# Optimization experiments

Measured on AMD Instinct MI355X. Metric: run time of the kernel, lower is better.

## Reference

```python
import jax, jax.numpy as jnp
import numpy as np

B, N, D = 8, 1024, 768
H, Y, M = 12, 64, 3072  # heads, head_dim, hopfield memories (4*D)
STEPS = 12
ALPHA = 0.1
EPS = 1e-5


def setup_inputs() -> dict:
    key = jax.random.key(0)
    k0, k1, k2, k3 = jax.random.split(key, 4)
    return {
        "x": jax.random.normal(k0, (B, N, D), dtype=jnp.float32),
        "gamma": jnp.ones((D,), dtype=jnp.float32),
        "beta_ln": jnp.zeros((D,), dtype=jnp.float32),
        "Wq": jax.random.normal(k1, (H, Y, D), dtype=jnp.float32) / np.float32(np.sqrt(D)),
        "Wk": jax.random.normal(k2, (H, Y, D), dtype=jnp.float32) / np.float32(np.sqrt(D)),
        "xi": jax.random.normal(k3, (M, D), dtype=jnp.float32) / np.float32(np.sqrt(D)),
    }


def _layernorm(x, gamma, beta_ln):
    mu = jnp.mean(x, axis=-1, keepdims=True)
    var = jnp.var(x, axis=-1, keepdims=True)
    return gamma * (x - mu) * jax.lax.rsqrt(var + EPS) + beta_ln


def _energy(g, Wq, Wk, xi):
    # Energy attention: E^ATT = -(1/beta) * sum_{h,q} logsumexp_k(beta * <K_hk, Q_hq>)
    q = jnp.einsum('hyd,bnd->bhny', Wq, g)
    k = jnp.einsum('hyd,bnd->bhny', Wk, g)
    beta = jnp.asarray(1.0 / np.sqrt(Y), g.dtype)
    scores = beta * jnp.einsum('bhky,bhqy->bhkq', k, q)  # [B,H,N_k,N_q]
    e_att = -(1.0 / beta) * jnp.sum(jax.nn.logsumexp(scores, axis=2))
    # Hopfield energy: E^HN = -0.5 * sum relu(g @ xi^T)^2
    h = jnp.einsum('bnd,md->bnm', g, xi)
    e_hn = -0.5 * jnp.sum(jnp.square(jax.nn.relu(h)))
    return e_att + e_hn


def reference(x, gamma, beta_ln, Wq, Wk, xi):
    grad_e = jax.grad(_energy)
    def step(xc, _):
        g = _layernorm(xc, gamma, beta_ln)
        # gradient taken at g (not chained through LayerNorm), then SGD update
        xc = xc - ALPHA * grad_e(g, Wq, Wk, xi)
        return xc, None
    out, _ = jax.lax.scan(step, x, None, length=STEPS)
    return out
```

## Files before the change

### kernel.cpp

```cpp
#include <hip/hip_runtime.h>
#include <math.h>

#define H_ 12
#define STEPS_ 12
#define ALPHA_ 0.1f
#define EPS_ 1e-5f
#define BETA_ 0.125f
#define NTOK 8192

typedef unsigned short u16;
typedef __attribute__((ext_vector_type(8))) u16 u16x8;
typedef __attribute__((ext_vector_type(4))) u16 u16x4;
typedef __attribute__((ext_vector_type(4))) float f32x4;
typedef __attribute__((ext_vector_type(8))) __bf16 bf16x8;

#define MFMA __builtin_amdgcn_mfma_f32_16x16x32_bf16

__device__ __forceinline__ u16 f2bf(float x) {
    unsigned u = __float_as_uint(x);
    u += 0x7FFFu + ((u >> 16) & 1u);
    return (u16)(u >> 16);
}
__device__ __forceinline__ float bf2f(u16 u) {
    return __uint_as_float(((unsigned)u) << 16);
}

__device__ __forceinline__ void gl2lds16(const u16* gsrc, u16* ldst) {
    __builtin_amdgcn_global_load_lds(
        (const __attribute__((address_space(1))) void*)gsrc,
        (__attribute__((address_space(3))) void*)ldst, 16, 0, 0);
}

#define RAW_BARRIER()   asm volatile("s_barrier" ::: "memory")
#define WAIT_VM(n)      asm volatile("s_waitcnt vmcnt(" #n ")" ::: "memory")
#define SCHED_FENCE()   __builtin_amdgcn_sched_barrier(0)

#define QUAD(IB, JB, BR) \
    { _Pragma("unroll") \
      for (int i_ = 0; i_ < 4; ++i_) { \
        _Pragma("unroll") \
        for (int j_ = 0; j_ < 2; ++j_) { \
            acc[(IB)+i_][(JB)+j_] = MFMA(afr[i_][0], BR[j_][0], acc[(IB)+i_][(JB)+j_], 0,0,0); \
            acc[(IB)+i_][(JB)+j_] = MFMA(afr[i_][1], BR[j_][1], acc[(IB)+i_][(JB)+j_], 0,0,0); \
        } } }

__global__ __launch_bounds__(256) void ln_kernel(const float* __restrict__ x,
    const float* __restrict__ gamma, const float* __restrict__ beta,
    u16* __restrict__ g)
{
    int row = blockIdx.x;
    const float* xr = x + (size_t)row * 768;
    u16* gr = g + (size_t)row * 768;
    int t = threadIdx.x;
    float v0 = xr[t], v1 = xr[t + 256], v2 = xr[t + 512];
    float s = v0 + v1 + v2;
    #pragma unroll
    for (int off = 32; off > 0; off >>= 1) s += __shfl_down(s, off);
    __shared__ float red[8];
    int wid = t >> 6, lane = t & 63;
    if (lane == 0) red[wid] = s;
    __syncthreads();
    if (t == 0) red[0] = (red[0] + red[1] + red[2] + red[3]) * (1.0f / 768.0f);
    __syncthreads();
    float mu = red[0];
    float d0 = v0 - mu, d1 = v1 - mu, d2 = v2 - mu;
    float ss = d0*d0 + d1*d1 + d2*d2;
    #pragma unroll
    for (int off = 32; off > 0; off >>= 1) ss += __shfl_down(ss, off);
    if (lane == 0) red[4 + wid] = ss;
    __syncthreads();
    if (t == 0) red[4] = rsqrtf((red[4] + red[5] + red[6] + red[7]) * (1.0f / 768.0f) + EPS_);
    __syncthreads();
    float rs = red[4];
    gr[t]       = f2bf(gamma[t]       * d0 * rs + beta[t]);
    gr[t + 256] = f2bf(gamma[t + 256] * d1 * rs + beta[t + 256]);
    gr[t + 512] = f2bf(gamma[t + 512] * d2 * rs + beta[t + 512]);
}

__global__ __launch_bounds__(192) void reduce_ln(const u16* __restrict__ part,
    float* __restrict__ xc, const float* __restrict__ gamma,
    const float* __restrict__ beta, u16* __restrict__ g)
{
    int row = blockIdx.x, t = threadIdx.x;
    const u16x4* p0 = (const u16x4*)(part + (size_t)row * 768);
    const u16x4* p1 = (const u16x4*)(part + (size_t)(8192 + row) * 768);
    const u16x4* p2 = (const u16x4*)(part + (size_t)(16384 + row) * 768);
    const u16x4* p3 = (const u16x4*)(part + (size_t)(24576 + row) * 768);
    f32x4* xr = (f32x4*)(xc + (size_t)row * 768);
    f32x4 v = xr[t];
    u16x4 a = p0[t], b = p1[t], c = p2[t], d4 = p3[t];
    #pragma unroll
    for (int e = 0; e < 4; ++e)
        v[e] = fmaf(ALPHA_, (bf2f(a[e]) + bf2f(b[e])) + (bf2f(c[e]) + bf2f(d4[e])), v[e]);
    xr[t] = v;
    float s = (v[0] + v[1]) + (v[2] + v[3]);
    #pragma unroll
    for (int off = 32; off > 0; off >>= 1) s += __shfl_down(s, off);
    __shared__ float red[8];
    int wid = t >> 6, lane = t & 63;
    if (lane == 0) red[wid] = s;
    __syncthreads();
    if (t == 0) red[0] = (red[0] + red[1] + red[2]) * (1.0f / 768.0f);
    __syncthreads();
    float mu = red[0];
    f32x4 d;
    #pragma unroll
    for (int e = 0; e < 4; ++e) d[e] = v[e] - mu;
    float ss = (d[0]*d[0] + d[1]*d[1]) + (d[2]*d[2] + d[3]*d[3]);
    #pragma unroll
    for (int off = 32; off > 0; off >>= 1) ss += __shfl_down(ss, off);
    if (lane == 0) red[4 + wid] = ss;
    __syncthreads();
    if (t == 0) red[4] = rsqrtf((red[4] + red[5] + red[6]) * (1.0f / 768.0f) + EPS_);
    __syncthreads();
    float rs = red[4];
    const f32x4 gm = *(const f32x4*)&gamma[t * 4];
    const f32x4 bt = *(const f32x4*)&beta[t * 4];
    u16x4 o;
    #pragma unroll
    for (int e = 0; e < 4; ++e) o[e] = f2bf(fmaf(gm[e], d[e] * rs, bt[e]));
    *(u16x4*)&g[(size_t)row * 768 + t * 4] = o;
}

__global__ __launch_bounds__(256) void convert_bf(const float* __restrict__ src,
                                                  u16* __restrict__ dst, int n4)
{
    int i = blockIdx.x * 256 + threadIdx.x;
    if (i < n4) {
        f32x4 v = *(const f32x4*)&src[i * 4];
        u16x4 o;
        #pragma unroll
        for (int e = 0; e < 4; ++e) o[e] = f2bf(v[e]);
        *(u16x4*)&dst[i * 4] = o;
    }
}

__global__ __launch_bounds__(256) void transpose_bf(const float* __restrict__ Wq,
    const float* __restrict__ Wk, const float* __restrict__ xi, u16* __restrict__ out)
{
    __shared__ float tile[64][65];
    int rb = blockIdx.x * 64, cb = blockIdx.y * 64;
    const float* src;
    if (rb < 768) src = Wq + (size_t)rb * 768;
    else if (rb < 1536) src = Wk + (size_t)(rb - 768) * 768;
    else src = xi + (size_t)(rb - 1536) * 768;
    int t = threadIdx.x;
    #pragma unroll
    for (int it = 0; it < 4; ++it) {
        int r = (t >> 4) + 16 * it;
        f32x4 v = *(const f32x4*)&src[(size_t)r * 768 + cb + (t & 15) * 4];
        #pragma unroll
        for (int e = 0; e < 4; ++e) tile[r][(t & 15) * 4 + e] = v[e];
    }
    __syncthreads();
    #pragma unroll
    for (int it = 0; it < 4; ++it) {
        int cl = (t >> 4) + 16 * it;
        u16x4 o;
        #pragma unroll
        for (int e = 0; e < 4; ++e) o[e] = f2bf(tile[(t & 15) * 4 + e][cl]);
        *(u16x4*)&out[(size_t)(cb + cl) * 4608 + rb + (t & 15) * 4] = o;
    }
}

__global__ __launch_bounds__(512) void gemm_fwd(
    const u16* __restrict__ A,
    const u16* __restrict__ Bt,
    u16* __restrict__ qkb, u16* __restrict__ qkT, u16* __restrict__ midb)
{
    __shared__ __align__(16) u16 S[2][32768];
    const int t = threadIdx.x, w = t >> 6, l = t & 63, g = l >> 4, cid = l & 15;
    const int lr = l & 15, lc = l >> 4;
    const int wm = w >> 2, wn = w & 3;
    const int flat = blockIdx.x;
    const int xcd = flat & 7, slot = flat >> 3;
    const int nid = slot >> 2, mloc = slot & 3;
    const int bm = (xcd * 4 + mloc) * 256;
    const int bn = nid * 256;
    const int NT = 12;

    const u16* aA[2]; const u16* bB[2];
    int ldA[2], ldB[2];
    #pragma unroll
    for (int hh = 0; hh < 2; ++hh) {
        aA[hh] = A  + (size_t)(bm + 16 * (hh * 8 + w) + lr) * 768 + 8 * lc;
        bB[hh] = Bt + (size_t)(bn + 16 * (hh * 8 + w) + lr) * 768 + 8 * lc;
        ldA[hh] = (128 * (hh * 8 + w) + l) * 8;
        ldB[hh] = 16384 + (128 * (hh * 8 + w) + l) * 8;
    }
    auto stageA = [&](int buf, int hh, int k0) {
        gl2lds16(aA[hh] + k0,      &S[buf][ldA[hh]]);
        gl2lds16(aA[hh] + k0 + 32, &S[buf][ldA[hh] + 512]);
    };
    auto stageB = [&](int buf, int hh, int k0) {
        gl2lds16(bB[hh] + k0,      &S[buf][ldB[hh]]);
        gl2lds16(bB[hh] + k0 + 32, &S[buf][ldB[hh] + 512]);
    };

    f32x4 acc[8][4] = {};
    bf16x8 afr[4][2], b0[2][2], b1[2][2];

    stageB(0, 0, 0); stageB(0, 1, 0); stageA(0, 0, 0); stageA(0, 1, 0);
    stageB(1, 0, 64); stageB(1, 1, 64);
    WAIT_VM(4); RAW_BARRIER();

    #pragma unroll 1
    for (int tt = 0; tt < NT; ++tt) {
        const int bf = tt & 1, ob = bf ^ 1;
        const u16* Sa = &S[bf][0];
        const u16* Sb = &S[bf][16384];
        #define LDS_A(ii, hh) (*(const bf16x8*)&Sa[(wm*1024 + (ii)*128 + (hh)*64 + l) * 8])
        #define LDS_B(jj, hh) (*(const bf16x8*)&Sb[((wn*4 + (jj))*128 + (hh)*64 + l) * 8])
        #pragma unroll
        for (int i = 0; i < 4; ++i) { afr[i][0] = LDS_A(i, 0); afr[i][1] = LDS_A(i, 1); }
        #pragma unroll
        for (int j = 0; j < 2; ++j) { b0[j][0] = LDS_B(j, 0); b0[j][1] = LDS_B(j, 1); }
        if (tt + 1 < NT) stageA(ob, 0, 64 * (tt + 1));
        RAW_BARRIER();
        __builtin_amdgcn_s_setprio(1);
        QUAD(0, 0, b0);
        __builtin_amdgcn_s_setprio(0);
        SCHED_FENCE(); RAW_BARRIER();
        #pragma unroll
        for (int j = 0; j < 2; ++j) { b1[j][0] = LDS_B(2 + j, 0); b1[j][1] = LDS_B(2 + j, 1); }
        if (tt + 1 < NT) stageA(ob, 1, 64 * (tt + 1));
        RAW_BARRIER();
        __builtin_amdgcn_s_setprio(1);
        QUAD(0, 2, b1);
        __builtin_amdgcn_s_setprio(0);
        SCHED_FENCE(); RAW_BARRIER();
        #pragma unroll
        for (int i = 0; i < 4; ++i) { afr[i][0] = LDS_A(4 + i, 0); afr[i][1] = LDS_A(4 + i, 1); }
        if (tt + 2 < NT) stageB(bf, 0, 64 * (tt + 2));
        RAW_BARRIER();
        __builtin_amdgcn_s_setprio(1);
        QUAD(4, 2, b1);
        __builtin_amdgcn_s_setprio(0);
        SCHED_FENCE(); RAW_BARRIER();
        if (tt + 2 < NT) stageB(bf, 1, 64 * (tt + 2));
        RAW_BARRIER();
        __builtin_amdgcn_s_setprio(1);
        QUAD(4, 0, b0);
        __builtin_amdgcn_s_setprio(0);
        SCHED_FENCE();
        if (tt < NT - 2)       { WAIT_VM(4); }
        else if (tt == NT - 2) { WAIT_VM(0); }
        RAW_BARRIER();
        #undef LDS_A
        #undef LDS_B
    }

    if (bn < 1536) {
        int bidx = bm >> 10;
        #pragma unroll
        for (int i = 0; i < 8; ++i) {
            int tok = bm + wm * 128 + 16 * i + 4 * g;
            #pragma unroll
            for (int j = 0; j < 4; ++j) {
                int col = bn + wn * 64 + 16 * j + cid;
                int sel = col >= 768 ? 1 : 0;
                int cc = col - 768 * sel;
                int hh = cc >> 6, yy = cc & 63;
                u16x4 tv;
                #pragma unroll
                for (int r = 0; r < 4; ++r) {
                    u16 bv = f2bf(acc[i][j][r]);
                    tv[r] = bv;
                    qkb[(size_t)(tok + r) * 1536 + col] = bv;
                }
                *(u16x4*)&qkT[((((size_t)bidx * 12 + hh) * 2 + sel) * 64 + yy) * 1024 + (tok & 1023)] = tv;
            }
        }
    } else {
        #pragma unroll
        for (int i = 0; i < 8; ++i)
            #pragma unroll
            for (int r = 0; r < 4; ++r) {
                size_t row = bm + wm * 128 + 16 * i + 4 * g + r;
                #pragma unroll
                for (int j = 0; j < 4; ++j) {
                    int col = bn + wn * 64 + 16 * j + cid;
                    midb[row * 4608 + col] = f2bf(fmaxf(acc[i][j][r], 0.0f));
                }
            }
    }
}

__global__ __launch_bounds__(512) void gemm_upd(
    const u16* __restrict__ A,
    const u16* __restrict__ Bt,
    u16* __restrict__ part)
{
    __shared__ __align__(16) u16 S[2][32768];
    const int t = threadIdx.x, w = t >> 6, l = t & 63, g = l >> 4, cid = l & 15;
    const int lr = l & 15, lc = l >> 4;
    const int wm = w >> 2, wn = w & 3;
    const int flat = blockIdx.x;
    const int xcd = flat & 7, slot = flat >> 3;
    const int z = slot / 12, rem = slot % 12;
    const int nid = rem >> 2, mloc = rem & 3;
    const int bm = (xcd * 4 + mloc) * 256, bn = nid * 256;
    const int kbeg = z * 1152;
    const int NT = 18;
    u16* out = part + (size_t)z * 8192 * 768;

    const u16* aA[2]; const u16* bB[2];
    int ldA[2], ldB[2];
    #pragma unroll
    for (int hh = 0; hh < 2; ++hh) {
        aA[hh] = A  + (size_t)(bm + 16 * (hh * 8 + w) + lr) * 4608 + kbeg + 8 * lc;
        bB[hh] = Bt + (size_t)(bn + 16 * (hh * 8 + w) + lr) * 4608 + kbeg + 8 * lc;
        ldA[hh] = (128 * (hh * 8 + w) + l) * 8;
        ldB[hh] = 16384 + (128 * (hh * 8 + w) + l) * 8;
    }
    auto stageA = [&](int buf, int hh, int k0) {
        gl2lds16(aA[hh] + k0,      &S[buf][ldA[hh]]);
        gl2lds16(aA[hh] + k0 + 32, &S[buf][ldA[hh] + 512]);
    };
    auto stageB = [&](int buf, int hh, int k0) {
        gl2lds16(bB[hh] + k0,      &S[buf][ldB[hh]]);
        gl2lds16(bB[hh] + k0 + 32, &S[buf][ldB[hh] + 512]);
    };

    f32x4 acc[8][4] = {};
    bf16x8 afr[4][2], b0[2][2], b1[2][2];

    stageB(0, 0, 0); stageB(0, 1, 0); stageA(0, 0, 0); stageA(0, 1, 0);
    stageB(1, 0, 64); stageB(1, 1, 64);
    WAIT_VM(4); RAW_BARRIER();

    #pragma unroll 1
    for (int tt = 0; tt < NT; ++tt) {
        const int bf = tt & 1, ob = bf ^ 1;
        const u16* Sa = &S[bf][0];
        const u16* Sb = &S[bf][16384];
        #define LDS_A(ii, hh) (*(const bf16x8*)&Sa[(wm*1024 + (ii)*128 + (hh)*64 + l) * 8])
        #define LDS_B(jj, hh) (*(const bf16x8*)&Sb[((wn*4 + (jj))*128 + (hh)*64 + l) * 8])
        #pragma unroll
        for (int i = 0; i < 4; ++i) { afr[i][0] = LDS_A(i, 0); afr[i][1] = LDS_A(i, 1); }
        #pragma unroll
        for (int j = 0; j < 2; ++j) { b0[j][0] = LDS_B(j, 0); b0[j][1] = LDS_B(j, 1); }
        if (tt + 1 < NT) stageA(ob, 0, 64 * (tt + 1));
        RAW_BARRIER();
        __builtin_amdgcn_s_setprio(1);
        QUAD(0, 0, b0);
        __builtin_amdgcn_s_setprio(0);
        SCHED_FENCE(); RAW_BARRIER();
        #pragma unroll
        for (int j = 0; j < 2; ++j) { b1[j][0] = LDS_B(2 + j, 0); b1[j][1] = LDS_B(2 + j, 1); }
        if (tt + 1 < NT) stageA(ob, 1, 64 * (tt + 1));
        RAW_BARRIER();
        __builtin_amdgcn_s_setprio(1);
        QUAD(0, 2, b1);
        __builtin_amdgcn_s_setprio(0);
        SCHED_FENCE(); RAW_BARRIER();
        #pragma unroll
        for (int i = 0; i < 4; ++i) { afr[i][0] = LDS_A(4 + i, 0); afr[i][1] = LDS_A(4 + i, 1); }
        if (tt + 2 < NT) stageB(bf, 0, 64 * (tt + 2));
        RAW_BARRIER();
        __builtin_amdgcn_s_setprio(1);
        QUAD(4, 2, b1);
        __builtin_amdgcn_s_setprio(0);
        SCHED_FENCE(); RAW_BARRIER();
        if (tt + 2 < NT) stageB(bf, 1, 64 * (tt + 2));
        RAW_BARRIER();
        __builtin_amdgcn_s_setprio(1);
        QUAD(4, 0, b0);
        __builtin_amdgcn_s_setprio(0);
        SCHED_FENCE();
        if (tt < NT - 2)       { WAIT_VM(4); }
        else if (tt == NT - 2) { WAIT_VM(0); }
        RAW_BARRIER();
        #undef LDS_A
        #undef LDS_B
    }

    #pragma unroll
    for (int i = 0; i < 8; ++i)
        #pragma unroll
        for (int r = 0; r < 4; ++r) {
            size_t row = bm + wm * 128 + 16 * i + 4 * g + r;
            #pragma unroll
            for (int j = 0; j < 4; ++j)
                out[row * 768 + bn + wn * 64 + 16 * j + cid] = f2bf(acc[i][j][r]);
        }
}

__global__ __launch_bounds__(256) void dq_kernel(const u16* __restrict__ qk,
    const u16* __restrict__ qkT, float* __restrict__ L, u16* __restrict__ mid)
{
    const int flat = blockIdx.x;
    const int xcd = flat & 7, slot = flat >> 3;
    const int bh = xcd * 12 + slot / 8;
    const int q0 = (slot % 8) << 7;
    const int b = bh / H_, h = bh % H_;
    const u16* qbase = qk + (size_t)b * 1024 * 1536 + h * 64;
    const u16* kbase = qbase + 768;
    const u16* ktg = qkT + ((size_t)bh * 2 + 1) * 64 * 1024;
    __shared__ __align__(16) u16 KB[2][8192];
    __shared__ __align__(16) u16 Ps[8192];
    const int t = threadIdx.x, w = t >> 6, l = t & 63, g = l >> 4, cid = l & 15;
    const int lr = l & 15, lc = l >> 4;

    #pragma unroll
    for (int h2 = 0; h2 < 2; ++h2)
        #pragma unroll
        for (int ch = 0; ch < 2; ++ch)
            gl2lds16(&qbase[(size_t)(q0 + 32 * w + 16 * h2 + lr) * 1536 + 32 * ch + 8 * lc],
                     &KB[0][(128 * (2 * w + h2) + 64 * ch + l) * 8]);
    __syncthreads();
    bf16x8 QF[2][2];
    #pragma unroll
    for (int jj = 0; jj < 2; ++jj)
        #pragma unroll
        for (int hh = 0; hh < 2; ++hh)
            QF[jj][hh] = *(const bf16x8*)&KB[0][(128 * (2 * w + jj) + 64 * hh + l) * 8];
    __syncthreads();

    auto stageK = [&](int buf, int kt) {
        #pragma unroll
        for (int ch = 0; ch < 2; ++ch) {
            gl2lds16(&kbase[(size_t)(kt * 64 + 16 * w + lr) * 1536 + 32 * ch + 8 * lc],
                     &KB[buf][(128 * w + 64 * ch + l) * 8]);
            gl2lds16(&ktg[(size_t)(16 * w + lr) * 1024 + kt * 64 + 32 * ch + 8 * lc],
                     &KB[buf][4096 + (128 * w + 64 * ch + l) * 8]);
        }
    };

    f32x4 acc[2][4] = {};
    float lrun[2] = {0.0f, 0.0f};

    stageK(0, 0); stageK(1, 1);
    #pragma unroll 1
    for (int kt = 0; kt < 16; ++kt) {
        if (kt == 15) { WAIT_VM(0); } else { WAIT_VM(4); }
        RAW_BARRIER();
        const int buf = kt & 1;
        const u16* Kn = &KB[buf][0];
        const u16* Kt = &KB[buf][4096];
        f32x4 s[4][2];
        #pragma unroll
        for (int i = 0; i < 4; ++i) {
            bf16x8 a0 = *(const bf16x8*)&Kn[(128 * i + l) * 8];
            bf16x8 a1 = *(const bf16x8*)&Kn[(128 * i + 64 + l) * 8];
            #pragma unroll
            for (int jj = 0; jj < 2; ++jj) {
                f32x4 z = {0.f, 0.f, 0.f, 0.f};
                z = MFMA(a0, QF[jj][0], z, 0, 0, 0);
                z = MFMA(a1, QF[jj][1], z, 0, 0, 0);
                s[i][jj] = z;
            }
        }
        #pragma unroll
        for (int jj = 0; jj < 2; ++jj) {
            float psum = 0.0f;
            #pragma unroll
            for (int i = 0; i < 4; ++i) {
                u16x4 pv;
                #pragma unroll
                for (int r = 0; r < 4; ++r) {
                    float p = __expf(s[i][jj][r] * BETA_);
                    psum += p;
                    pv[r] = f2bf(p);
                }
                *(u16x4*)&Ps[(128 * (2 * w + jj) + 32 * i + 16 * (g >> 1) + cid) * 8 + 4 * (g & 1)] = pv;
            }
            psum += __shfl_xor(psum, 16);
            psum += __shfl_xor(psum, 32);
            lrun[jj] += psum;
        }
        #pragma unroll
        for (int jj = 0; jj < 2; ++jj) {
            bf16x8 p0 = *(const bf16x8*)&Ps[(128 * (2 * w + jj) + l) * 8];
            bf16x8 p1 = *(const bf16x8*)&Ps[(128 * (2 * w + jj) + 64 + l) * 8];
            #pragma unroll
            for (int j = 0; j < 4; ++j) {
                acc[jj][j] = MFMA(p0, *(const bf16x8*)&Kt[(128 * j + l) * 8], acc[jj][j], 0, 0, 0);
                acc[jj][j] = MFMA(p1, *(const bf16x8*)&Kt[(128 * j + 64 + l) * 8], acc[jj][j], 0, 0, 0);
            }
        }
        RAW_BARRIER();
        if (kt + 2 < 16) stageK(buf, kt + 2);
    }
    #pragma unroll
    for (int jj = 0; jj < 2; ++jj) {
        if (g == 0)
            L[(size_t)bh * 1024 + q0 + 32 * w + 16 * jj + cid] = __logf(lrun[jj]);
        float linv = 1.0f / lrun[jj];
        #pragma unroll
        for (int r = 0; r < 4; ++r) {
            float fr = __shfl(linv, 4 * g + r);
            int row = q0 + 32 * w + 16 * jj + 4 * g + r;
            #pragma unroll
            for (int j = 0; j < 4; ++j)
                mid[(size_t)(b * 1024 + row) * 4608 + h * 64 + 16 * j + cid] = f2bf(acc[jj][j][r] * fr);
        }
    }
}

__global__ __launch_bounds__(256) void dk_kernel(const u16* __restrict__ qk,
    const u16* __restrict__ qkT, const float* __restrict__ L, u16* __restrict__ mid)
{
    const int flat = blockIdx.x;
    const int xcd = flat & 7, slot = flat >> 3;
    const int bh = xcd * 12 + slot / 8;
    const int k0 = (slot % 8) << 7;
    const int b = bh / H_, h = bh % H_;
    const u16* qbase = qk + (size_t)b * 1024 * 1536 + h * 64;
    const u16* kbase = qbase + 768;
    const u16* qtg = qkT + ((size_t)bh * 2 + 0) * 64 * 1024;
    __shared__ __align__(16) u16 KB[2][8192];
    __shared__ __align__(16) u16 Ps[8192];
    const int t = threadIdx.x, w = t >> 6, l = t & 63, g = l >> 4, cid = l & 15;
    const int lr = l & 15, lc = l >> 4;

    #pragma unroll
    for (int h2 = 0; h2 < 2; ++h2)
        #pragma unroll
        for (int ch = 0; ch < 2; ++ch)
            gl2lds16(&kbase[(size_t)(k0 + 32 * w + 16 * h2 + lr) * 1536 + 32 * ch + 8 * lc],
                     &KB[0][(128 * (2 * w + h2) + 64 * ch + l) * 8]);
    __syncthreads();
    bf16x8 KF[2][2];
    #pragma unroll
    for (int jj = 0; jj < 2; ++jj)
        #pragma unroll
        for (int hh = 0; hh < 2; ++hh)
            KF[jj][hh] = *(const bf16x8*)&KB[0][(128 * (2 * w + jj) + 64 * hh + l) * 8];
    __syncthreads();

    auto stageQ = [&](int buf, int qt) {
        #pragma unroll
        for (int ch = 0; ch < 2; ++ch) {
            gl2lds16(&qbase[(size_t)(qt * 64 + 16 * w + lr) * 1536 + 32 * ch + 8 * lc],
                     &KB[buf][(128 * w + 64 * ch + l) * 8]);
            gl2lds16(&qtg[(size_t)(16 * w + lr) * 1024 + qt * 64 + 32 * ch + 8 * lc],
                     &KB[buf][4096 + (128 * w + 64 * ch + l) * 8]);
        }
    };

    f32x4 acc[2][4] = {};
    stageQ(0, 0); stageQ(1, 1);
    #pragma unroll 1
    for (int qt = 0; qt < 16; ++qt) {
        if (qt == 15) { WAIT_VM(0); } else { WAIT_VM(4); }
        RAW_BARRIER();
        const int buf = qt & 1;
        const u16* Qn = &KB[buf][0];
        const u16* Qt = &KB[buf][4096];
        #pragma unroll
        for (int i = 0; i < 4; ++i) {
            bf16x8 a0 = *(const bf16x8*)&Qn[(128 * i + l) * 8];
            bf16x8 a1 = *(const bf16x8*)&Qn[(128 * i + 64 + l) * 8];
            f32x4 lv = *(const f32x4*)&L[(size_t)bh * 1024 + qt * 64 + 16 * i + 4 * g];
            #pragma unroll
            for (int jj = 0; jj < 2; ++jj) {
                f32x4 z = {0.f, 0.f, 0.f, 0.f};
                z = MFMA(a0, KF[jj][0], z, 0, 0, 0);
                z = MFMA(a1, KF[jj][1], z, 0, 0, 0);
                u16x4 pv;
                #pragma unroll
                for (int r = 0; r < 4; ++r)
                    pv[r] = f2bf(__expf(fmaf(z[r], BETA_, -lv[r])));
                *(u16x4*)&Ps[(128 * (2 * w + jj) + 32 * i + 16 * (g >> 1) + cid) * 8 + 4 * (g & 1)] = pv;
            }
        }
        #pragma unroll
        for (int jj = 0; jj < 2; ++jj) {
            bf16x8 p0 = *(const bf16x8*)&Ps[(128 * (2 * w + jj) + l) * 8];
            bf16x8 p1 = *(const bf16x8*)&Ps[(128 * (2 * w + jj) + 64 + l) * 8];
            #pragma unroll
            for (int j = 0; j < 4; ++j) {
                acc[jj][j] = MFMA(p0, *(const bf16x8*)&Qt[(128 * j + l) * 8], acc[jj][j], 0, 0, 0);
                acc[jj][j] = MFMA(p1, *(const bf16x8*)&Qt[(128 * j + 64 + l) * 8], acc[jj][j], 0, 0, 0);
            }
        }
        RAW_BARRIER();
        if (qt + 2 < 16) stageQ(buf, qt + 2);
    }
    #pragma unroll
    for (int jj = 0; jj < 2; ++jj)
        #pragma unroll
        for (int r = 0; r < 4; ++r) {
            int row = k0 + 32 * w + 16 * jj + 4 * g + r;
            #pragma unroll
            for (int j = 0; j < 4; ++j)
                mid[(size_t)(b * 1024 + row) * 4608 + 768 + h * 64 + 16 * j + cid] = f2bf(acc[jj][j][r]);
        }
}

extern "C" void kernel_launch(void* const* d_in, const int* in_sizes, int n_in,
                              void* d_out, int out_size, void* d_ws, size_t ws_size,
                              hipStream_t stream)
{
    const float* x     = (const float*)d_in[0];
    const float* gamma = (const float*)d_in[1];
    const float* betap = (const float*)d_in[2];
    const float* Wq    = (const float*)d_in[3];
    const float* Wk    = (const float*)d_in[4];
    const float* xi    = (const float*)d_in[5];
    float* xc = (float*)d_out;

    char* p = (char*)d_ws;
    u16* wcat_bf  = (u16*)p; p += (size_t)4608 * 768 * 2;
    u16* wcatT_bf = (u16*)p; p += (size_t)768 * 4608 * 2;
    u16* g_bf     = (u16*)p; p += (size_t)NTOK * 768 * 2;
    u16* qk_bf    = (u16*)p; p += (size_t)NTOK * 1536 * 2;
    u16* qkT_bf   = (u16*)p; p += (size_t)96 * 2 * 64 * 1024 * 2;
    u16* mid_bf   = (u16*)p; p += (size_t)NTOK * 4608 * 2;
    float* L      = (float*)p; p += (size_t)96 * 1024 * 4;
    u16* part = qk_bf;
    (void)ws_size; (void)in_sizes; (void)n_in; (void)out_size;

    hipMemcpyAsync(xc, x, (size_t)NTOK * 768 * 4, hipMemcpyDeviceToDevice, stream);

    convert_bf<<<576, 256, 0, stream>>>(Wq, wcat_bf, 147456);
    convert_bf<<<576, 256, 0, stream>>>(Wk, wcat_bf + 768 * 768, 147456);
    convert_bf<<<2304, 256, 0, stream>>>(xi, wcat_bf + 2 * 768 * 768, 589824);
    transpose_bf<<<dim3(72, 12), 256, 0, stream>>>(Wq, Wk, xi, wcatT_bf);

    ln_kernel<<<NTOK, 256, 0, stream>>>(x, gamma, betap, g_bf);

    for (int step = 0; step < STEPS_; ++step) {
        gemm_fwd<<<576, 512, 0, stream>>>(
            g_bf, wcat_bf, qk_bf, qkT_bf, mid_bf);
        dq_kernel<<<768, 256, 0, stream>>>(qk_bf, qkT_bf, L, mid_bf);
        dk_kernel<<<768, 256, 0, stream>>>(qk_bf, qkT_bf, L, mid_bf);
        gemm_upd<<<384, 512, 0, stream>>>(mid_bf, wcatT_bf, part);
        reduce_ln<<<NTOK, 192, 0, stream>>>(part, xc, gamma, betap, g_bf);
    }
}
```

Before: 3.359 ms.

## Retile GEMMs to 256x192 blocks and halve split-K partials in update GEMM

Both the forward and update GEMMs switch from 256x256 to 256x192 output tiles, rebalancing the block count (768 forward blocks, 256 update blocks) so it divides evenly over the CUs and cuts shared memory per block. The update GEMM also moves from 4-way to 2-way split-K with a longer K loop, so reduce_ln reads and sums only two bf16 partial buffers. The staging and MFMA schedule is rewritten for three B fragments per wave. The price is less parallelism per K slice in the update GEMM and a lower compute-to-load ratio per tile.

After: 3.116 ms. -7.2%, faster.

```diff
diff --git a/kernel.cpp b/kernel.cpp
--- a/kernel.cpp
+++ b/kernel.cpp
@@ -35,15 +35,6 @@
 #define WAIT_VM(n)      asm volatile("s_waitcnt vmcnt(" #n ")" ::: "memory")
 #define SCHED_FENCE()   __builtin_amdgcn_sched_barrier(0)
 
-#define QUAD(IB, JB, BR) \
-    { _Pragma("unroll") \
-      for (int i_ = 0; i_ < 4; ++i_) { \
-        _Pragma("unroll") \
-        for (int j_ = 0; j_ < 2; ++j_) { \
-            acc[(IB)+i_][(JB)+j_] = MFMA(afr[i_][0], BR[j_][0], acc[(IB)+i_][(JB)+j_], 0,0,0); \
-            acc[(IB)+i_][(JB)+j_] = MFMA(afr[i_][1], BR[j_][1], acc[(IB)+i_][(JB)+j_], 0,0,0); \
-        } } }
-
 __global__ __launch_bounds__(256) void ln_kernel(const float* __restrict__ x,
     const float* __restrict__ gamma, const float* __restrict__ beta,
     u16* __restrict__ g)
@@ -84,14 +75,11 @@
     int row = blockIdx.x, t = threadIdx.x;
     const u16x4* p0 = (const u16x4*)(part + (size_t)row * 768);
     const u16x4* p1 = (const u16x4*)(part + (size_t)(8192 + row) * 768);
-    const u16x4* p2 = (const u16x4*)(part + (size_t)(16384 + row) * 768);
-    const u16x4* p3 = (const u16x4*)(part + (size_t)(24576 + row) * 768);
     f32x4* xr = (f32x4*)(xc + (size_t)row * 768);
     f32x4 v = xr[t];
-    u16x4 a = p0[t], b = p1[t], c = p2[t], d4 = p3[t];
-    #pragma unroll
-    for (int e = 0; e < 4; ++e)
-        v[e] = fmaf(ALPHA_, (bf2f(a[e]) + bf2f(b[e])) + (bf2f(c[e]) + bf2f(d4[e])), v[e]);
+    u16x4 a = p0[t], b = p1[t];
+    #pragma unroll
+    for (int e = 0; e < 4; ++e) v[e] = fmaf(ALPHA_, bf2f(a[e]) + bf2f(b[e]), v[e]);
     xr[t] = v;
     float s = (v[0] + v[1]) + (v[2] + v[3]);
     #pragma unroll
@@ -163,12 +151,13 @@
     }
 }
 
+
 __global__ __launch_bounds__(512) void gemm_fwd(
     const u16* __restrict__ A,
     const u16* __restrict__ Bt,
     u16* __restrict__ qkb, u16* __restrict__ qkT, u16* __restrict__ midb)
 {
-    __shared__ __align__(16) u16 S[2][32768];
+    __shared__ __align__(16) u16 S[2][28672];
     const int t = threadIdx.x, w = t >> 6, l = t & 63, g = l >> 4, cid = l & 15;
     const int lr = l & 15, lc = l >> 4;
     const int wm = w >> 2, wn = w & 3;
@@ -176,78 +165,89 @@
     const int xcd = flat & 7, slot = flat >> 3;
     const int nid = slot >> 2, mloc = slot & 3;
     const int bm = (xcd * 4 + mloc) * 256;
-    const int bn = nid * 256;
+    const int bn = nid * 192;
     const int NT = 12;
 
-    const u16* aA[2]; const u16* bB[2];
-    int ldA[2], ldB[2];
-    #pragma unroll
-    for (int hh = 0; hh < 2; ++hh) {
-        aA[hh] = A  + (size_t)(bm + 16 * (hh * 8 + w) + lr) * 768 + 8 * lc;
-        bB[hh] = Bt + (size_t)(bn + 16 * (hh * 8 + w) + lr) * 768 + 8 * lc;
-        ldA[hh] = (128 * (hh * 8 + w) + l) * 8;
-        ldB[hh] = 16384 + (128 * (hh * 8 + w) + l) * 8;
-    }
-    auto stageA = [&](int buf, int hh, int k0) {
-        gl2lds16(aA[hh] + k0,      &S[buf][ldA[hh]]);
-        gl2lds16(aA[hh] + k0 + 32, &S[buf][ldA[hh] + 512]);
-    };
-    auto stageB = [&](int buf, int hh, int k0) {
-        gl2lds16(bB[hh] + k0,      &S[buf][ldB[hh]]);
-        gl2lds16(bB[hh] + k0 + 32, &S[buf][ldB[hh] + 512]);
-    };
-
-    f32x4 acc[8][4] = {};
-    bf16x8 afr[4][2], b0[2][2], b1[2][2];
-
-    stageB(0, 0, 0); stageB(0, 1, 0); stageA(0, 0, 0); stageA(0, 1, 0);
-    stageB(1, 0, 64); stageB(1, 1, 64);
-    WAIT_VM(4); RAW_BARRIER();
+    const u16* aS[4]; int ldA[4];
+    #pragma unroll
+    for (int j = 0; j < 4; ++j) {
+        int rf = 2 * w + (j >> 1), kh = j & 1;
+        aS[j] = A + (size_t)(bm + 16 * rf + lr) * 768 + 32 * kh + 8 * lc;
+        ldA[j] = rf * 1024 + kh * 512 + l * 8;
+    }
+    const u16* bS[3]; int ldB[3];
+    #pragma unroll
+    for (int j = 0; j < 3; ++j) {
+        int c = 3 * w + j, rf = c >> 1, kh = c & 1;
+        bS[j] = Bt + (size_t)(bn + 16 * rf + lr) * 768 + 32 * kh + 8 * lc;
+        ldB[j] = 16384 + rf * 1024 + kh * 512 + l * 8;
+    }
+
+    f32x4 acc[8][3] = {};
+    bf16x8 afr[4][2], b0[2][2], b1[2];
+
+    #pragma unroll
+    for (int j = 0; j < 3; ++j) gl2lds16(bS[j], &S[0][ldB[j]]);
+    #pragma unroll
+    for (int j = 0; j < 4; ++j) gl2lds16(aS[j], &S[0][ldA[j]]);
+    #pragma unroll
+    for (int j = 0; j < 3; ++j) gl2lds16(bS[j] + 64, &S[1][ldB[j]]);
+    WAIT_VM(3); RAW_BARRIER();
 
     #pragma unroll 1
     for (int tt = 0; tt < NT; ++tt) {
         const int bf = tt & 1, ob = bf ^ 1;
         const u16* Sa = &S[bf][0];
         const u16* Sb = &S[bf][16384];
-        #define LDS_A(ii, hh) (*(const bf16x8*)&Sa[(wm*1024 + (ii)*128 + (hh)*64 + l) * 8])
-        #define LDS_B(jj, hh) (*(const bf16x8*)&Sb[((wn*4 + (jj))*128 + (hh)*64 + l) * 8])
+        #define LDS_A(ii, hh) (*(const bf16x8*)&Sa[((wm * 8 + (ii)) * 128 + (hh) * 64 + l) * 8])
+        #define LDS_B(jj, hh) (*(const bf16x8*)&Sb[((3 * wn + (jj)) * 128 + (hh) * 64 + l) * 8])
+        #define MM(ii, jj, BF0, BF1) { \
+            acc[ii][jj] = MFMA(afr[(ii) & 3][0], BF0, acc[ii][jj], 0, 0, 0); \
+            acc[ii][jj] = MFMA(afr[(ii) & 3][1], BF1, acc[ii][jj], 0, 0, 0); }
         #pragma unroll
         for (int i = 0; i < 4; ++i) { afr[i][0] = LDS_A(i, 0); afr[i][1] = LDS_A(i, 1); }
         #pragma unroll
         for (int j = 0; j < 2; ++j) { b0[j][0] = LDS_B(j, 0); b0[j][1] = LDS_B(j, 1); }
-        if (tt + 1 < NT) stageA(ob, 0, 64 * (tt + 1));
-        RAW_BARRIER();
-        __builtin_amdgcn_s_setprio(1);
-        QUAD(0, 0, b0);
+        if (tt + 1 < NT) { gl2lds16(aS[0] + 64 * (tt + 1), &S[ob][ldA[0]]);
+                           gl2lds16(aS[1] + 64 * (tt + 1), &S[ob][ldA[1]]); }
+        RAW_BARRIER();
+        __builtin_amdgcn_s_setprio(1);
+        #pragma unroll
+        for (int i = 0; i < 4; ++i) { MM(i, 0, b0[0][0], b0[0][1]); MM(i, 1, b0[1][0], b0[1][1]); }
         __builtin_amdgcn_s_setprio(0);
         SCHED_FENCE(); RAW_BARRIER();
-        #pragma unroll
-        for (int j = 0; j < 2; ++j) { b1[j][0] = LDS_B(2 + j, 0); b1[j][1] = LDS_B(2 + j, 1); }
-        if (tt + 1 < NT) stageA(ob, 1, 64 * (tt + 1));
-        RAW_BARRIER();
-        __builtin_amdgcn_s_setprio(1);
-        QUAD(0, 2, b1);
+        b1[0] = LDS_B(2, 0); b1[1] = LDS_B(2, 1);
+        if (tt + 1 < NT) { gl2lds16(aS[2] + 64 * (tt + 1), &S[ob][ldA[2]]);
+                           gl2lds16(aS[3] + 64 * (tt + 1), &S[ob][ldA[3]]); }
+        RAW_BARRIER();
+        __builtin_amdgcn_s_setprio(1);
+        #pragma unroll
+        for (int i = 0; i < 4; ++i) { MM(i, 2, b1[0], b1[1]); }
         __builtin_amdgcn_s_setprio(0);
         SCHED_FENCE(); RAW_BARRIER();
         #pragma unroll
         for (int i = 0; i < 4; ++i) { afr[i][0] = LDS_A(4 + i, 0); afr[i][1] = LDS_A(4 + i, 1); }
-        if (tt + 2 < NT) stageB(bf, 0, 64 * (tt + 2));
-        RAW_BARRIER();
-        __builtin_amdgcn_s_setprio(1);
-        QUAD(4, 2, b1);
+        if (tt + 2 < NT) { gl2lds16(bS[0] + 64 * (tt + 2), &S[bf][ldB[0]]);
+                           gl2lds16(bS[1] + 64 * (tt + 2), &S[bf][ldB[1]]); }
+        RAW_BARRIER();
+        __builtin_amdgcn_s_setprio(1);
+        #pragma unroll
+        for (int i = 0; i < 4; ++i) { MM(4 + i, 2, b1[0], b1[1]); }
         __builtin_amdgcn_s_setprio(0);
         SCHED_FENCE(); RAW_BARRIER();
-        if (tt + 2 < NT) stageB(bf, 1, 64 * (tt + 2));
-        RAW_BARRIER();
-        __builtin_amdgcn_s_setprio(1);
-        QUAD(4, 0, b0);
+        if (tt + 2 < NT) gl2lds16(bS[2] + 64 * (tt + 2), &S[bf][ldB[2]]);
+        RAW_BARRIER();
+        __builtin_amdgcn_s_setprio(1);
+        #pragma unroll
+        for (int i = 0; i < 4; ++i) { MM(4 + i, 0, b0[0][0], b0[0][1]); MM(4 + i, 1, b0[1][0], b0[1][1]); }
         __builtin_amdgcn_s_setprio(0);
         SCHED_FENCE();
-        if (tt < NT - 2)       { WAIT_VM(4); }
+        if (tt < NT - 2)       { WAIT_VM(3); }
         else if (tt == NT - 2) { WAIT_VM(0); }
         RAW_BARRIER();
         #undef LDS_A
         #undef LDS_B
+        #undef MM
     }
 
     if (bn < 1536) {
@@ -256,8 +256,8 @@
         for (int i = 0; i < 8; ++i) {
             int tok = bm + wm * 128 + 16 * i + 4 * g;
             #pragma unroll
-            for (int j = 0; j < 4; ++j) {
-                int col = bn + wn * 64 + 16 * j + cid;
+            for (int j = 0; j < 3; ++j) {
+                int col = bn + wn * 48 + 16 * j + cid;
                 int sel = col >= 768 ? 1 : 0;
                 int cc = col - 768 * sel;
                 int hh = cc >> 6, yy = cc & 63;
@@ -278,8 +278,8 @@
             for (int r = 0; r < 4; ++r) {
                 size_t row = bm + wm * 128 + 16 * i + 4 * g + r;
                 #pragma unroll
-                for (int j = 0; j < 4; ++j) {
-                    int col = bn + wn * 64 + 16 * j + cid;
+                for (int j = 0; j < 3; ++j) {
+                    int col = bn + wn * 48 + 16 * j + cid;
                     midb[row * 4608 + col] = f2bf(fmaxf(acc[i][j][r], 0.0f));
                 }
             }
@@ -291,88 +291,99 @@
     const u16* __restrict__ Bt,
     u16* __restrict__ part)
 {
-    __shared__ __align__(16) u16 S[2][32768];
+    __shared__ __align__(16) u16 S[2][28672];
     const int t = threadIdx.x, w = t >> 6, l = t & 63, g = l >> 4, cid = l & 15;
     const int lr = l & 15, lc = l >> 4;
     const int wm = w >> 2, wn = w & 3;
     const int flat = blockIdx.x;
     const int xcd = flat & 7, slot = flat >> 3;
-    const int z = slot / 12, rem = slot % 12;
+    const int z = slot >> 4, rem = slot & 15;
     const int nid = rem >> 2, mloc = rem & 3;
-    const int bm = (xcd * 4 + mloc) * 256, bn = nid * 256;
-    const int kbeg = z * 1152;
-    const int NT = 18;
+    const int bm = (xcd * 4 + mloc) * 256, bn = nid * 192;
+    const int kbeg = z * 2304;
+    const int NT = 36;
     u16* out = part + (size_t)z * 8192 * 768;
 
-    const u16* aA[2]; const u16* bB[2];
-    int ldA[2], ldB[2];
-    #pragma unroll
-    for (int hh = 0; hh < 2; ++hh) {
-        aA[hh] = A  + (size_t)(bm + 16 * (hh * 8 + w) + lr) * 4608 + kbeg + 8 * lc;
-        bB[hh] = Bt + (size_t)(bn + 16 * (hh * 8 + w) + lr) * 4608 + kbeg + 8 * lc;
-        ldA[hh] = (128 * (hh * 8 + w) + l) * 8;
-        ldB[hh] = 16384 + (128 * (hh * 8 + w) + l) * 8;
-    }
-    auto stageA = [&](int buf, int hh, int k0) {
-        gl2lds16(aA[hh] + k0,      &S[buf][ldA[hh]]);
-        gl2lds16(aA[hh] + k0 + 32, &S[buf][ldA[hh] + 512]);
-    };
-    auto stageB = [&](int buf, int hh, int k0) {
-        gl2lds16(bB[hh] + k0,      &S[buf][ldB[hh]]);
-        gl2lds16(bB[hh] + k0 + 32, &S[buf][ldB[hh] + 512]);
-    };
-
-    f32x4 acc[8][4] = {};
-    bf16x8 afr[4][2], b0[2][2], b1[2][2];
-
-    stageB(0, 0, 0); stageB(0, 1, 0); stageA(0, 0, 0); stageA(0, 1, 0);
-    stageB(1, 0, 64); stageB(1, 1, 64);
-    WAIT_VM(4); RAW_BARRIER();
+    const u16* aS[4]; int ldA[4];
+    #pragma unroll
+    for (int j = 0; j < 4; ++j) {
+        int rf = 2 * w + (j >> 1), kh = j & 1;
+        aS[j] = A + (size_t)(bm + 16 * rf + lr) * 4608 + kbeg + 32 * kh + 8 * lc;
+        ldA[j] = rf * 1024 + kh * 512 + l * 8;
+    }
+    const u16* bS[3]; int ldB[3];
+    #pragma unroll
+    for (int j = 0; j < 3; ++j) {
+        int c = 3 * w + j, rf = c >> 1, kh = c & 1;
+        bS[j] = Bt + (size_t)(bn + 16 * rf + lr) * 4608 + kbeg + 32 * kh + 8 * lc;
+        ldB[j] = 16384 + rf * 1024 + kh * 512 + l * 8;
+    }
+
+    f32x4 acc[8][3] = {};
+    bf16x8 afr[4][2], b0[2][2], b1[2];
+
+    #pragma unroll
+    for (int j = 0; j < 3; ++j) gl2lds16(bS[j], &S[0][ldB[j]]);
+    #pragma unroll
+    for (int j = 0; j < 4; ++j) gl2lds16(aS[j], &S[0][ldA[j]]);
+    #pragma unroll
+    for (int j = 0; j < 3; ++j) gl2lds16(bS[j] + 64, &S[1][ldB[j]]);
+    WAIT_VM(3); RAW_BARRIER();
 
     #pragma unroll 1
     for (int tt = 0; tt < NT; ++tt) {
         const int bf = tt & 1, ob = bf ^ 1;
         const u16* Sa = &S[bf][0];
         const u16* Sb = &S[bf][16384];
-        #define LDS_A(ii, hh) (*(const bf16x8*)&Sa[(wm*1024 + (ii)*128 + (hh)*64 + l) * 8])
-        #define LDS_B(jj, hh) (*(const bf16x8*)&Sb[((wn*4 + (jj))*128 + (hh)*64 + l) * 8])
+        #define LDS_A(ii, hh) (*(const bf16x8*)&Sa[((wm * 8 + (ii)) * 128 + (hh) * 64 + l) * 8])
+        #define LDS_B(jj, hh) (*(const bf16x8*)&Sb[((3 * wn + (jj)) * 128 + (hh) * 64 + l) * 8])
+        #define MM(ii, jj, BF0, BF1) { \
+            acc[ii][jj] = MFMA(afr[(ii) & 3][0], BF0, acc[ii][jj], 0, 0, 0); \
+            acc[ii][jj] = MFMA(afr[(ii) & 3][1], BF1, acc[ii][jj], 0, 0, 0); }
         #pragma unroll
         for (int i = 0; i < 4; ++i) { afr[i][0] = LDS_A(i, 0); afr[i][1] = LDS_A(i, 1); }
         #pragma unroll
         for (int j = 0; j < 2; ++j) { b0[j][0] = LDS_B(j, 0); b0[j][1] = LDS_B(j, 1); }
-        if (tt + 1 < NT) stageA(ob, 0, 64 * (tt + 1));
-        RAW_BARRIER();
-        __builtin_amdgcn_s_setprio(1);
-        QUAD(0, 0, b0);
+        if (tt + 1 < NT) { gl2lds16(aS[0] + 64 * (tt + 1), &S[ob][ldA[0]]);
+                           gl2lds16(aS[1] + 64 * (tt + 1), &S[ob][ldA[1]]); }
+        RAW_BARRIER();
+        __builtin_amdgcn_s_setprio(1);
+        #pragma unroll
+        for (int i = 0; i < 4; ++i) { MM(i, 0, b0[0][0], b0[0][1]); MM(i, 1, b0[1][0], b0[1][1]); }
         __builtin_amdgcn_s_setprio(0);
         SCHED_FENCE(); RAW_BARRIER();
-        #pragma unroll
-        for (int j = 0; j < 2; ++j) { b1[j][0] = LDS_B(2 + j, 0); b1[j][1] = LDS_B(2 + j, 1); }
-        if (tt + 1 < NT) stageA(ob, 1, 64 * (tt + 1));
-        RAW_BARRIER();
-        __builtin_amdgcn_s_setprio(1);
-        QUAD(0, 2, b1);
+        b1[0] = LDS_B(2, 0); b1[1] = LDS_B(2, 1);
+        if (tt + 1 < NT) { gl2lds16(aS[2] + 64 * (tt + 1), &S[ob][ldA[2]]);
+                           gl2lds16(aS[3] + 64 * (tt + 1), &S[ob][ldA[3]]); }
+        RAW_BARRIER();
+        __builtin_amdgcn_s_setprio(1);
+        #pragma unroll
+        for (int i = 0; i < 4; ++i) { MM(i, 2, b1[0], b1[1]); }
         __builtin_amdgcn_s_setprio(0);
         SCHED_FENCE(); RAW_BARRIER();
         #pragma unroll
         for (int i = 0; i < 4; ++i) { afr[i][0] = LDS_A(4 + i, 0); afr[i][1] = LDS_A(4 + i, 1); }
-        if (tt + 2 < NT) stageB(bf, 0, 64 * (tt + 2));
-        RAW_BARRIER();
-        __builtin_amdgcn_s_setprio(1);
-        QUAD(4, 2, b1);
+        if (tt + 2 < NT) { gl2lds16(bS[0] + 64 * (tt + 2), &S[bf][ldB[0]]);
+                           gl2lds16(bS[1] + 64 * (tt + 2), &S[bf][ldB[1]]); }
+        RAW_BARRIER();
+        __builtin_amdgcn_s_setprio(1);
+        #pragma unroll
+        for (int i = 0; i < 4; ++i) { MM(4 + i, 2, b1[0], b1[1]); }
         __builtin_amdgcn_s_setprio(0);
         SCHED_FENCE(); RAW_BARRIER();
-        if (tt + 2 < NT) stageB(bf, 1, 64 * (tt + 2));
-        RAW_BARRIER();
-        __builtin_amdgcn_s_setprio(1);
-        QUAD(4, 0, b0);
+        if (tt + 2 < NT) gl2lds16(bS[2] + 64 * (tt + 2), &S[bf][ldB[2]]);
+        RAW_BARRIER();
+        __builtin_amdgcn_s_setprio(1);
+        #pragma unroll
+        for (int i = 0; i < 4; ++i) { MM(4 + i, 0, b0[0][0], b0[0][1]); MM(4 + i, 1, b0[1][0], b0[1][1]); }
         __builtin_amdgcn_s_setprio(0);
         SCHED_FENCE();
-        if (tt < NT - 2)       { WAIT_VM(4); }
+        if (tt < NT - 2)       { WAIT_VM(3); }
         else if (tt == NT - 2) { WAIT_VM(0); }
         RAW_BARRIER();
         #undef LDS_A
         #undef LDS_B
+        #undef MM
     }
 
     #pragma unroll
@@ -381,8 +392,8 @@
         for (int r = 0; r < 4; ++r) {
             size_t row = bm + wm * 128 + 16 * i + 4 * g + r;
             #pragma unroll
-            for (int j = 0; j < 4; ++j)
-                out[row * 768 + bn + wn * 64 + 16 * j + cid] = f2bf(acc[i][j][r]);
+            for (int j = 0; j < 3; ++j)
+                out[row * 768 + bn + wn * 48 + 16 * j + cid] = f2bf(acc[i][j][r]);
         }
 }
 
@@ -622,11 +633,11 @@
     ln_kernel<<<NTOK, 256, 0, stream>>>(x, gamma, betap, g_bf);
 
     for (int step = 0; step < STEPS_; ++step) {
-        gemm_fwd<<<576, 512, 0, stream>>>(
+        gemm_fwd<<<768, 512, 0, stream>>>(
             g_bf, wcat_bf, qk_bf, qkT_bf, mid_bf);
         dq_kernel<<<768, 256, 0, stream>>>(qk_bf, qkT_bf, L, mid_bf);
         dk_kernel<<<768, 256, 0, stream>>>(qk_bf, qkT_bf, L, mid_bf);
-        gemm_upd<<<384, 512, 0, stream>>>(mid_bf, wcatT_bf, part);
+        gemm_upd<<<256, 512, 0, stream>>>(mid_bf, wcatT_bf, part);
         reduce_ln<<<NTOK, 192, 0, stream>>>(part, xc, gamma, betap, g_bf);
     }
 }
```
